# Kernel tuning notes

Hardware: AMD Instinct MI355X
Metric: run time of the kernel (lower is better)

## Reference

```python
import jax, jax.numpy as jnp
import numpy as np
from functools import partial

DN = ('NCHW', 'OIHW', 'NCHW')

def _conv(x, w):
    # 'same' conv, stride 1, NCHW
    return jax.lax.conv_general_dilated(x, w, window_strides=(1, 1),
                                        padding='SAME', dimension_numbers=DN)

def setup_inputs() -> dict:
    key = jax.random.key(0)
    ks = jax.random.split(key, 5)
    B, T, Cin, Oh, H, Wd = 8, 16, 64, 64, 56, 56
    x = jax.random.normal(ks[0], (B, T, Cin, H, Wd), dtype=jnp.float32)
    h = jax.random.normal(ks[1], (B, Oh, H, Wd), dtype=jnp.float32)
    # xavier-uniform-ish init scale for 3x3 kernels
    def xavier(k, shape):
        fan_in = shape[1] * shape[2] * shape[3]
        fan_out = shape[0] * shape[2] * shape[3]
        a = float(np.sqrt(6.0 / (fan_in + fan_out)))
        return jax.random.uniform(k, shape, dtype=jnp.float32, minval=-a, maxval=a)
    W = xavier(ks[2], (3 * Oh, Cin, 3, 3))  # [Wz; Wr; Wc]
    U = xavier(ks[3], (2 * Oh, Oh, 3, 3))   # [Uz; Ur]
    C = xavier(ks[4], (Oh, Oh, 3, 3))       # Uc (on r*h)
    return {"x": x, "h": h, "W": W, "U": U, "C": C}

def reference(x, h, W, U, C):
    Oh = C.shape[0]
    xt_major = jnp.swapaxes(x, 0, 1)  # [T, B, Cin, H, W]

    def step(h, xt):
        wx = _conv(xt, W)             # [B, 3*Oh, H, W]
        uh = _conv(h, U)              # [B, 2*Oh, H, W]
        z = jax.nn.sigmoid(wx[:, :Oh] + uh[:, :Oh])            # update gate
        r = jax.nn.sigmoid(wx[:, Oh:2 * Oh] + uh[:, Oh:2 * Oh])  # reset gate
        h_tilde = jnp.tanh(wx[:, 2 * Oh:] + _conv(r * h, C))
        h_new = (1.0 - z) * h + z * h_tilde
        return h_new, h_new

    h_last, outs = jax.lax.scan(step, h, xt_major)
    return jnp.swapaxes(outs, 0, 1), h_last  # [B, T, Oh, H, W], [B, Oh, H, W]
```

## Files before the change

### kernel.cpp

```cpp
#include <hip/hip_runtime.h>
#include <math.h>


#define PIX 4224
#define PIMG 244992
#define BIMG ((size_t)8 * PIMG)
#define WXS ((size_t)5505024)
#define HL_OFF ((size_t)25690112)
#define SLOT 2176

typedef unsigned short u16;
typedef __attribute__((ext_vector_type(8))) __bf16 bf16x8;
typedef __attribute__((ext_vector_type(4))) float f32x4;

__device__ __forceinline__ float bf2f(u16 u) {
  unsigned v = ((unsigned)u) << 16;
  float f;
  __builtin_memcpy(&f, &v, 4);
  return f;
}
__device__ __forceinline__ u16 f2bf(float f) {
  unsigned u;
  __builtin_memcpy(&u, &f, 4);
  u = (u + 0x7FFFu + ((u >> 16) & 1u)) >> 16;
  return (u16)u;
}
__device__ __forceinline__ void gll16(const u16* g, u16* l) {
  __builtin_amdgcn_global_load_lds(
      (const __attribute__((address_space(1))) void*)g,
      (__attribute__((address_space(3))) void*)l, 16, 0, 0);
}

__device__ __forceinline__ void stage_row(const u16* img, int prow, int x0,
                                          u16* ring, int slot, int lane,
                                          int wv) {
  const u16* g = img + (size_t)prow * PIX + x0 * 64;
  u16* l = ring + slot * SLOT;
  gll16(g + wv * 512 + lane * 8, l + wv * 512);
  if (wv == 0 && lane < 16) gll16(g + 2048 + lane * 8, l + 2048);
}

__device__ __forceinline__ void loadB18(const u16* wr, int NCH,
                                        bf16x8 (&B)[6][3]) {
#pragma unroll
  for (int p = 0; p < 6; ++p) {
    const int ky = p >> 1, kc = p & 1;
#pragma unroll
    for (int kx = 0; kx < 3; ++kx)
      B[p][kx] = *(const bf16x8*)(wr + (size_t)((ky * 3 + kx) * NCH) * 64 +
                                  kc * 32);
  }
}

__device__ __forceinline__ void conv_unit(const u16* ring, int rcb,
                                          const bf16x8 (&B)[6][3],
                                          f32x4 (&acc)[2], int lane) {
#pragma unroll
  for (int p = 0; p < 6; ++p) {
    const int ky = p >> 1, kc = p & 1;
    const int slot = (rcb + ky) & 7;
    bf16x8 af[2][3];
#pragma unroll
    for (int mf = 0; mf < 2; ++mf)
#pragma unroll
      for (int kx = 0; kx < 3; ++kx) {
        const int pp = mf * 16 + (lane & 15) + kx;
        const int sl = (kc * 4 + (lane >> 4)) ^ (pp & 7);
        af[mf][kx] = *(const bf16x8*)(ring + slot * SLOT + pp * 64 + sl * 8);
      }
#pragma unroll
    for (int kx = 0; kx < 3; ++kx)
#pragma unroll
      for (int mf = 0; mf < 2; ++mf)
        acc[mf] = __builtin_amdgcn_mfma_f32_16x16x32_bf16(af[mf][kx], B[p][kx],
                                                          acc[mf], 0, 0, 0);
  }
}

#define UNIT_SYNC() \
  asm volatile("s_waitcnt vmcnt(0)" ::: "memory"); \
  __syncthreads();

__device__ __forceinline__ void do_convW(const u16* __restrict__ xslot,
                                         const u16* __restrict__ wcat,
                                         u16* __restrict__ wx, int id,
                                         u16* ring) {
  const int ns = id / 112;
  const int rem = id % 112;
  const int b = rem & 7;
  const int v = rem >> 3;
  const int x0 = (v & 1) * 32;
  const int y0 = (v >> 1) * 8;
  const int lane = threadIdx.x & 63, wv = threadIdx.x >> 6;
  const int n0 = ns * 64 + wv * 16;

  const u16* wr = wcat + (size_t)(n0 + (lane & 15)) * 64 + (lane >> 4) * 8;
  bf16x8 B[6][3];
  loadB18(wr, 192, B);

  const u16* img = xslot + (size_t)b * PIMG;
#pragma unroll
  for (int k = 0; k < 3; ++k) stage_row(img, y0 + k, x0, ring, k, lane, wv);

  int S = 3;
#pragma unroll
  for (int u = 0; u < 8; ++u) {
    UNIT_SYNC();
    const int tgt = (u + 1 < 8) ? (u + 3) : 2;
#pragma unroll
    for (; S <= tgt; ++S)
      stage_row(img, y0 + S, x0, ring, S & 7, lane, wv);

    f32x4 acc[2] = {{0.f, 0.f, 0.f, 0.f}, {0.f, 0.f, 0.f, 0.f}};
    conv_unit(ring, u, B, acc, lane);

    const int y = y0 + u;
    const size_t rowb = ((size_t)(b * 56) + y) * 64;
    const int n = n0 + (lane & 15);
#pragma unroll
    for (int mf = 0; mf < 2; ++mf)
#pragma unroll
      for (int r = 0; r < 4; ++r) {
        const int px = x0 + mf * 16 + 4 * (lane >> 4) + r;
        wx[(rowb + px) * 192 + n] = f2bf(acc[mf][r]);
      }
  }
}

__device__ __forceinline__ void xprep_row(const float* __restrict__ x,
                                          u16* __restrict__ dst, int t, int b,
                                          int y, float (*tx)[57]) {
  const int tid = threadIdx.x;
  for (int i = tid; i < 64 * 56; i += 256) {
    int ci = i / 56, px = i % 56;
    tx[ci][px] = x[((size_t)(b * 16 + t) * 64 + ci) * 3136 + y * 56 + px];
  }
  __syncthreads();
  const size_t pb = (size_t)b * PIMG + (size_t)(y + 1) * PIX;
  for (int i = tid; i < 56 * 64; i += 256) {
    int px = i / 64, ci = i % 64;
    int gx = px + 1;
    dst[pb + gx * 64 + (((ci >> 3) ^ (gx & 7)) << 3) + (ci & 7)] =
        f2bf(tx[ci][px]);
  }
}

__global__ __launch_bounds__(256) void wprep_k(const float* __restrict__ W,
                                               const float* __restrict__ U,
                                               const float* __restrict__ C,
                                               u16* __restrict__ wcat) {
  int i = blockIdx.x * 256 + threadIdx.x;
  if (i >= 221184) return;
  float v;
  if (i < 110592) {
    int plane = i / 12288, rem = i % 12288, o = rem / 64, ci = rem % 64;
    v = W[(size_t)(o * 64 + ci) * 9 + plane];
  } else if (i < 184320) {
    int j = i - 110592;
    int plane = j / 8192, rem = j % 8192, o = rem / 64, ci = rem % 64;
    v = U[(size_t)(o * 64 + ci) * 9 + plane];
  } else {
    int j = i - 184320;
    int plane = j / 4096, rem = j % 4096, o = rem / 64, ci = rem % 64;
    v = C[(size_t)(o * 64 + ci) * 9 + plane];
  }
  wcat[i] = f2bf(v);
}

__global__ __launch_bounds__(256) void hinit_k(const float* __restrict__ h,
                                               u16* __restrict__ hpad,
                                               _Float16* __restrict__ hstate) {
  __shared__ float t[64][57];
  const int y = blockIdx.x, b = blockIdx.y;
  const int tid = threadIdx.x;
  for (int i = tid; i < 64 * 56; i += 256) {
    int ci = i / 56, xx = i % 56;
    t[ci][xx] = h[((size_t)(b * 64) + ci) * 3136 + y * 56 + xx];
  }
  __syncthreads();
  const size_t pb = (size_t)b * PIMG + (size_t)(y + 1) * PIX;
  const size_t sb = ((size_t)(b * 56) + y) * 64;
  for (int i = tid; i < 56 * 64; i += 256) {
    int px = i / 64, ci = i % 64;
    float v = t[ci][px];
    int gx = px + 1;
    hpad[pb + gx * 64 + (((ci >> 3) ^ (gx & 7)) << 3) + (ci & 7)] = f2bf(v);
    hstate[(sb + px) * 64 + ci] = (_Float16)v;
  }
}

__global__ __launch_bounds__(256) void xprep01_k(const float* __restrict__ x,
                                                 u16* __restrict__ x0,
                                                 u16* __restrict__ x1) {
  __shared__ float tt[64][57];
  const int t = blockIdx.y;
  xprep_row(x, t ? x1 : x0, t, blockIdx.x & 7, blockIdx.x >> 3, tt);
}

__global__ __launch_bounds__(256, 3) void convW0_k(const u16* __restrict__ xs,
                                                   const u16* __restrict__ wcat,
                                                   u16* __restrict__ wx) {
  __shared__ __align__(16) u16 ring[8 * SLOT];
  do_convW(xs, wcat, wx, blockIdx.x, ring);
}

__global__ __launch_bounds__(256, 3) void convUW_k(
    const u16* __restrict__ hpad, const u16* __restrict__ xpad_n,
    const u16* __restrict__ wcat, const u16* __restrict__ wx_c,
    u16* __restrict__ wx_n, _Float16* __restrict__ zbuf,
    u16* __restrict__ rhpad) {
  __shared__ __align__(16) u16 ring[8 * SLOT];
  const int bid = blockIdx.x;
  if (bid >= 448) {
    do_convW(xpad_n, wcat, wx_n, bid - 448, ring);
    return;
  }
  const int ns = bid / 224;
  const int rem = bid % 224;
  const int b = rem & 7;
  const int r2 = rem >> 3;
  const int x0 = (r2 & 1) * 32;
  const int y0 = (r2 >> 1) * 4;
  const int lane = threadIdx.x & 63, wv = threadIdx.x >> 6;
  const int n0 = ns * 64 + wv * 16;

  const u16* wr =
      wcat + 110592 + (size_t)(n0 + (lane & 15)) * 64 + (lane >> 4) * 8;
  bf16x8 B[6][3];
  loadB18(wr, 128, B);

  const u16* img = hpad + (size_t)b * PIMG;
#pragma unroll
  for (int k = 0; k < 3; ++k) stage_row(img, y0 + k, x0, ring, k, lane, wv);

  int S = 3;
#pragma unroll
  for (int u = 0; u < 4; ++u) {
    UNIT_SYNC();
    const int tgt = (u + 1 < 4) ? (u + 3) : 2;
#pragma unroll
    for (; S <= tgt; ++S)
      stage_row(img, y0 + S, x0, ring, S & 7, lane, wv);

    f32x4 acc[2] = {{0.f, 0.f, 0.f, 0.f}, {0.f, 0.f, 0.f, 0.f}};
    conv_unit(ring, u, B, acc, lane);

    const int y = y0 + u;
    const size_t rowb = ((size_t)(b * 56) + y) * 64;
    const int n = n0 + (lane & 15);
#pragma unroll
    for (int mf = 0; mf < 2; ++mf)
#pragma unroll
      for (int r = 0; r < 4; ++r) {
        const int px = x0 + mf * 16 + 4 * (lane >> 4) + r;
        if (px < 56) {
          const float a = bf2f(wx_c[(rowb + px) * 192 + n]) + acc[mf][r];
          const float s = 1.f / (1.f + __expf(-a));
          if (ns == 0) {
            zbuf[(rowb + px) * 64 + n] = (_Float16)s;
          } else {
            const int ci = n - 64;
            const int cp = mf * 16 + 4 * (lane >> 4) + r + 1;
            const int slotc = (u + 1) & 7;
            const float hv =
                bf2f(ring[slotc * SLOT + cp * 64 +
                          (((ci >> 3) ^ (cp & 7)) << 3) + (ci & 7)]);
            const int gx = px + 1;
            rhpad[(size_t)b * PIMG + (size_t)(y + 1) * PIX + gx * 64 +
                  (((ci >> 3) ^ (gx & 7)) << 3) + (ci & 7)] = f2bf(s * hv);
          }
        }
      }
  }
}

__global__ __launch_bounds__(256, 3) void convCX_k(
    const float* __restrict__ x, u16* __restrict__ xpad_w,
    const u16* __restrict__ rhpad, const u16* __restrict__ wcat,
    const u16* __restrict__ wx_c, const _Float16* __restrict__ zbuf,
    _Float16* __restrict__ hstate, u16* __restrict__ hpad,
    float* __restrict__ out, int t) {
  __shared__ __align__(16) u16 ring[8 * SLOT];
  __shared__ float ldt[4][16][33];
  const int bid = blockIdx.x;
  if (bid >= 448) {
    const int id = bid - 448;
    xprep_row(x, xpad_w, t + 2, id & 7, id >> 3, (float(*)[57])ring);
    return;
  }
  const int b = bid & 7;
  const int r2 = bid >> 3;
  const int x0 = (r2 & 1) * 32;
  const int y0 = (r2 >> 1) * 2;
  const int lane = threadIdx.x & 63, wv = threadIdx.x >> 6;
  const int n0 = wv * 16;

  const u16* wr =
      wcat + 184320 + (size_t)(n0 + (lane & 15)) * 64 + (lane >> 4) * 8;
  bf16x8 B[6][3];
  loadB18(wr, 64, B);

  const u16* img = rhpad + (size_t)b * PIMG;
#pragma unroll
  for (int k = 0; k < 3; ++k) stage_row(img, y0 + k, x0, ring, k, lane, wv);

#pragma unroll
  for (int u = 0; u < 2; ++u) {
    UNIT_SYNC();
    if (u == 0) stage_row(img, y0 + 3, x0, ring, 3, lane, wv);

    f32x4 acc[2] = {{0.f, 0.f, 0.f, 0.f}, {0.f, 0.f, 0.f, 0.f}};
    conv_unit(ring, u, B, acc, lane);

    const int y = y0 + u;
    const size_t rowb = ((size_t)(b * 56) + y) * 64;
    const int n = n0 + (lane & 15);
    float hnv[2][4];
#pragma unroll
    for (int mf = 0; mf < 2; ++mf)
#pragma unroll
      for (int r = 0; r < 4; ++r) {
        const int px = x0 + mf * 16 + 4 * (lane >> 4) + r;
        hnv[mf][r] = 0.f;
        if (px < 56) {
          const float a = bf2f(wx_c[(rowb + px) * 192 + 128 + n]) + acc[mf][r];
          const float htil = tanhf(a);
          const float z = (float)zbuf[(rowb + px) * 64 + n];
          const float ho = (float)hstate[(rowb + px) * 64 + n];
          const float hn = fmaf(z, htil - ho, ho);
          hstate[(rowb + px) * 64 + n] = (_Float16)hn;
          const int gx = px + 1;
          hpad[(size_t)b * PIMG + (size_t)(y + 1) * PIX + gx * 64 +
               (((n >> 3) ^ (gx & 7)) << 3) + (n & 7)] = f2bf(hn);
          hnv[mf][r] = hn;
        }
      }
    __syncthreads();
#pragma unroll
    for (int mf = 0; mf < 2; ++mf)
#pragma unroll
      for (int r = 0; r < 4; ++r)
        ldt[wv][lane & 15][mf * 16 + 4 * (lane >> 4) + r] = hnv[mf][r];
    __syncthreads();
    const int xl = lane & 31;
    const int px = x0 + xl;
    if (px < 56) {
#pragma unroll
      for (int cc = 0; cc < 8; ++cc) {
        const int ch = (lane >> 5) * 8 + cc;
        const float v = ldt[wv][ch][xl];
        out[(((size_t)(b * 16 + t)) * 64 + n0 + ch) * 3136 + y * 56 + px] = v;
        if (t == 15)
          out[HL_OFF + ((size_t)(b * 64) + n0 + ch) * 3136 + y * 56 + px] = v;
      }
    }
  }
}

extern "C" void kernel_launch(void* const* d_in, const int* in_sizes, int n_in,
                              void* d_out, int out_size, void* d_ws,
                              size_t ws_size, hipStream_t stream) {
  const float* x = (const float*)d_in[0];
  const float* h = (const float*)d_in[1];
  const float* W = (const float*)d_in[2];
  const float* U = (const float*)d_in[3];
  const float* C = (const float*)d_in[4];
  float* out = (float*)d_out;

  u16* ws_u = (u16*)d_ws;
  u16* xpad = ws_u;
  u16* hpad = xpad + 2 * BIMG;
  u16* rhpad = hpad + BIMG;
  u16* wcat = rhpad + BIMG;
  u16* wxr = wcat + 221184;
  _Float16* zbuf = (_Float16*)(wxr + 2 * WXS);
  _Float16* hstate = zbuf + 1835008;

  hipMemsetAsync(d_ws, 0, (size_t)4 * BIMG * sizeof(u16), stream);
  wprep_k<<<864, 256, 0, stream>>>(W, U, C, wcat);
  hinit_k<<<dim3(56, 8), 256, 0, stream>>>(h, hpad, hstate);
  xprep01_k<<<dim3(448, 2), 256, 0, stream>>>(x, xpad, xpad + BIMG);
  convW0_k<<<336, 256, 0, stream>>>(xpad, wcat, wxr);

  for (int t = 0; t < 16; ++t) {
    u16* xn = xpad + (size_t)((t + 1) & 1) * BIMG;
    u16* xw = xpad + (size_t)(t & 1) * BIMG;
    const u16* wxc = wxr + (size_t)(t & 1) * WXS;
    u16* wxn = wxr + (size_t)((t + 1) & 1) * WXS;

    const int nbA = 448 + ((t < 15) ? 336 : 0);
    convUW_k<<<nbA, 256, 0, stream>>>(hpad, xn, wcat, wxc, wxn, zbuf, rhpad);

    const int nbB = 448 + ((t < 14) ? 448 : 0);
    convCX_k<<<nbB, 256, 0, stream>>>(x, xw, rhpad, wcat, wxc, zbuf, hstate,
                                      hpad, out, t);
  }
}
```

Measured before the change: 813.7 us.

## Stage full padded rows and give each wave a 32x32 output tile

Conv blocks now stage whole padded image rows (both x halves) into a 4-slot LDS ring instead of half-width rows in an 8-slot ring. Each wave computes two 16-channel N fragments over a 32-pixel half, doubling the MFMA work per A-fragment load, and grid sizes are halved to match. The goal is to cut redundant halo loads and LDS A-fragment reads per MFMA. In exchange each wave holds twice as many weight registers, and occupancy drops to 2 blocks per CU with fewer blocks per launch. This could hurt latency hiding and SM fill, especially for the small convCX grid.

```diff
diff --git a/kernel.cpp b/kernel.cpp
--- a/kernel.cpp
+++ b/kernel.cpp
@@ -7,7 +7,7 @@
 #define BIMG ((size_t)8 * PIMG)
 #define WXS ((size_t)5505024)
 #define HL_OFF ((size_t)25690112)
-#define SLOT 2176
+#define SLOTW 4224
 
 typedef unsigned short u16;
 typedef __attribute__((ext_vector_type(8))) __bf16 bf16x8;
@@ -31,49 +31,54 @@
       (__attribute__((address_space(3))) void*)l, 16, 0, 0);
 }
 
-__device__ __forceinline__ void stage_row(const u16* img, int prow, int x0,
-                                          u16* ring, int slot, int lane,
-                                          int wv) {
-  const u16* g = img + (size_t)prow * PIX + x0 * 64;
-  u16* l = ring + slot * SLOT;
-  gll16(g + wv * 512 + lane * 8, l + wv * 512);
-  if (wv == 0 && lane < 16) gll16(g + 2048 + lane * 8, l + 2048);
-}
-
-__device__ __forceinline__ void loadB18(const u16* wr, int NCH,
-                                        bf16x8 (&B)[6][3]) {
+__device__ __forceinline__ void stage_rowf(const u16* img, int prow, u16* ring,
+                                           int slot, int lane, int wv) {
+  const u16* g = img + (size_t)prow * PIX;
+  u16* l = ring + slot * SLOTW;
+#pragma unroll
+  for (int c = wv; c < 8; c += 4) gll16(g + c * 512 + lane * 8, l + c * 512);
+  if (wv == 3 && lane < 16) gll16(g + 4096 + lane * 8, l + 4096);
+}
+
+__device__ __forceinline__ void loadB36(const u16* wr, int NCH,
+                                        bf16x8 (&B)[6][3][2]) {
 #pragma unroll
   for (int p = 0; p < 6; ++p) {
     const int ky = p >> 1, kc = p & 1;
 #pragma unroll
     for (int kx = 0; kx < 3; ++kx)
-      B[p][kx] = *(const bf16x8*)(wr + (size_t)((ky * 3 + kx) * NCH) * 64 +
-                                  kc * 32);
-  }
-}
-
-__device__ __forceinline__ void conv_unit(const u16* ring, int rcb,
-                                          const bf16x8 (&B)[6][3],
-                                          f32x4 (&acc)[2], int lane) {
+#pragma unroll
+      for (int nf = 0; nf < 2; ++nf)
+        B[p][kx][nf] = *(const bf16x8*)(wr + (size_t)((ky * 3 + kx) * NCH) * 64 +
+                                        nf * 1024 + kc * 32);
+  }
+}
+
+__device__ __forceinline__ void conv_unit2(const u16* ring, int rcb,
+                                           const bf16x8 (&B)[6][3][2],
+                                           f32x4 (&acc)[2][2], int lane,
+                                           int x0w) {
 #pragma unroll
   for (int p = 0; p < 6; ++p) {
     const int ky = p >> 1, kc = p & 1;
-    const int slot = (rcb + ky) & 7;
+    const int slot = (rcb + ky) & 3;
     bf16x8 af[2][3];
 #pragma unroll
     for (int mf = 0; mf < 2; ++mf)
 #pragma unroll
       for (int kx = 0; kx < 3; ++kx) {
-        const int pp = mf * 16 + (lane & 15) + kx;
+        const int pp = x0w + mf * 16 + (lane & 15) + kx;
         const int sl = (kc * 4 + (lane >> 4)) ^ (pp & 7);
-        af[mf][kx] = *(const bf16x8*)(ring + slot * SLOT + pp * 64 + sl * 8);
+        af[mf][kx] = *(const bf16x8*)(ring + slot * SLOTW + pp * 64 + sl * 8);
       }
 #pragma unroll
     for (int kx = 0; kx < 3; ++kx)
 #pragma unroll
       for (int mf = 0; mf < 2; ++mf)
-        acc[mf] = __builtin_amdgcn_mfma_f32_16x16x32_bf16(af[mf][kx], B[p][kx],
-                                                          acc[mf], 0, 0, 0);
+#pragma unroll
+        for (int nf = 0; nf < 2; ++nf)
+          acc[mf][nf] = __builtin_amdgcn_mfma_f32_16x16x32_bf16(
+              af[mf][kx], B[p][kx][nf], acc[mf][nf], 0, 0, 0);
   }
 }
 
@@ -85,44 +90,46 @@
                                          const u16* __restrict__ wcat,
                                          u16* __restrict__ wx, int id,
                                          u16* ring) {
-  const int ns = id / 112;
-  const int rem = id % 112;
+  const int ns = id / 56;
+  const int rem = id % 56;
   const int b = rem & 7;
-  const int v = rem >> 3;
-  const int x0 = (v & 1) * 32;
-  const int y0 = (v >> 1) * 8;
+  const int y0 = (rem >> 3) * 8;
   const int lane = threadIdx.x & 63, wv = threadIdx.x >> 6;
-  const int n0 = ns * 64 + wv * 16;
-
-  const u16* wr = wcat + (size_t)(n0 + (lane & 15)) * 64 + (lane >> 4) * 8;
-  bf16x8 B[6][3];
-  loadB18(wr, 192, B);
+  const int chs = wv & 1, x0w = (wv >> 1) * 32;
+  const int nb = ns * 64 + chs * 32;
+
+  const u16* wr = wcat + (size_t)(nb + (lane & 15)) * 64 + (lane >> 4) * 8;
+  bf16x8 B[6][3][2];
+  loadB36(wr, 192, B);
 
   const u16* img = xslot + (size_t)b * PIMG;
 #pragma unroll
-  for (int k = 0; k < 3; ++k) stage_row(img, y0 + k, x0, ring, k, lane, wv);
-
-  int S = 3;
+  for (int k = 0; k < 3; ++k) stage_rowf(img, y0 + k, ring, k, lane, wv);
+
 #pragma unroll
   for (int u = 0; u < 8; ++u) {
     UNIT_SYNC();
-    const int tgt = (u + 1 < 8) ? (u + 3) : 2;
-#pragma unroll
-    for (; S <= tgt; ++S)
-      stage_row(img, y0 + S, x0, ring, S & 7, lane, wv);
-
-    f32x4 acc[2] = {{0.f, 0.f, 0.f, 0.f}, {0.f, 0.f, 0.f, 0.f}};
-    conv_unit(ring, u, B, acc, lane);
+    if (u < 7) stage_rowf(img, y0 + u + 3, ring, (u + 3) & 3, lane, wv);
+
+    f32x4 acc[2][2];
+#pragma unroll
+    for (int mf = 0; mf < 2; ++mf)
+#pragma unroll
+      for (int nf = 0; nf < 2; ++nf) acc[mf][nf] = (f32x4){0.f, 0.f, 0.f, 0.f};
+    conv_unit2(ring, u, B, acc, lane, x0w);
 
     const int y = y0 + u;
     const size_t rowb = ((size_t)(b * 56) + y) * 64;
-    const int n = n0 + (lane & 15);
-#pragma unroll
-    for (int mf = 0; mf < 2; ++mf)
-#pragma unroll
-      for (int r = 0; r < 4; ++r) {
-        const int px = x0 + mf * 16 + 4 * (lane >> 4) + r;
-        wx[(rowb + px) * 192 + n] = f2bf(acc[mf][r]);
+#pragma unroll
+    for (int mf = 0; mf < 2; ++mf)
+#pragma unroll
+      for (int nf = 0; nf < 2; ++nf) {
+        const int n = nb + nf * 16 + (lane & 15);
+#pragma unroll
+        for (int r = 0; r < 4; ++r) {
+          const int px = x0w + mf * 16 + 4 * (lane >> 4) + r;
+          wx[(rowb + px) * 192 + n] = f2bf(acc[mf][nf][r]);
+        }
       }
   }
 }
@@ -197,161 +204,173 @@
   xprep_row(x, t ? x1 : x0, t, blockIdx.x & 7, blockIdx.x >> 3, tt);
 }
 
-__global__ __launch_bounds__(256, 3) void convW0_k(const u16* __restrict__ xs,
+__global__ __launch_bounds__(256, 2) void convW0_k(const u16* __restrict__ xs,
                                                    const u16* __restrict__ wcat,
                                                    u16* __restrict__ wx) {
-  __shared__ __align__(16) u16 ring[8 * SLOT];
+  __shared__ __align__(16) u16 ring[4 * SLOTW];
   do_convW(xs, wcat, wx, blockIdx.x, ring);
 }
 
-__global__ __launch_bounds__(256, 3) void convUW_k(
+__global__ __launch_bounds__(256, 2) void convUW_k(
     const u16* __restrict__ hpad, const u16* __restrict__ xpad_n,
     const u16* __restrict__ wcat, const u16* __restrict__ wx_c,
     u16* __restrict__ wx_n, _Float16* __restrict__ zbuf,
     u16* __restrict__ rhpad) {
-  __shared__ __align__(16) u16 ring[8 * SLOT];
+  __shared__ __align__(16) u16 ring[4 * SLOTW];
   const int bid = blockIdx.x;
-  if (bid >= 448) {
-    do_convW(xpad_n, wcat, wx_n, bid - 448, ring);
+  if (bid >= 224) {
+    do_convW(xpad_n, wcat, wx_n, bid - 224, ring);
     return;
   }
-  const int ns = bid / 224;
-  const int rem = bid % 224;
+  const int ns = bid / 112;
+  const int rem = bid % 112;
   const int b = rem & 7;
-  const int r2 = rem >> 3;
-  const int x0 = (r2 & 1) * 32;
-  const int y0 = (r2 >> 1) * 4;
+  const int y0 = (rem >> 3) * 4;
   const int lane = threadIdx.x & 63, wv = threadIdx.x >> 6;
-  const int n0 = ns * 64 + wv * 16;
+  const int chs = wv & 1, x0w = (wv >> 1) * 32;
+  const int nb = ns * 64 + chs * 32;
 
   const u16* wr =
-      wcat + 110592 + (size_t)(n0 + (lane & 15)) * 64 + (lane >> 4) * 8;
-  bf16x8 B[6][3];
-  loadB18(wr, 128, B);
+      wcat + 110592 + (size_t)(nb + (lane & 15)) * 64 + (lane >> 4) * 8;
+  bf16x8 B[6][3][2];
+  loadB36(wr, 128, B);
 
   const u16* img = hpad + (size_t)b * PIMG;
 #pragma unroll
-  for (int k = 0; k < 3; ++k) stage_row(img, y0 + k, x0, ring, k, lane, wv);
-
-  int S = 3;
+  for (int k = 0; k < 3; ++k) stage_rowf(img, y0 + k, ring, k, lane, wv);
+
 #pragma unroll
   for (int u = 0; u < 4; ++u) {
     UNIT_SYNC();
-    const int tgt = (u + 1 < 4) ? (u + 3) : 2;
-#pragma unroll
-    for (; S <= tgt; ++S)
-      stage_row(img, y0 + S, x0, ring, S & 7, lane, wv);
-
-    f32x4 acc[2] = {{0.f, 0.f, 0.f, 0.f}, {0.f, 0.f, 0.f, 0.f}};
-    conv_unit(ring, u, B, acc, lane);
+    if (u < 3) stage_rowf(img, y0 + u + 3, ring, (u + 3) & 3, lane, wv);
+
+    f32x4 acc[2][2];
+#pragma unroll
+    for (int mf = 0; mf < 2; ++mf)
+#pragma unroll
+      for (int nf = 0; nf < 2; ++nf) acc[mf][nf] = (f32x4){0.f, 0.f, 0.f, 0.f};
+    conv_unit2(ring, u, B, acc, lane, x0w);
 
     const int y = y0 + u;
     const size_t rowb = ((size_t)(b * 56) + y) * 64;
-    const int n = n0 + (lane & 15);
-#pragma unroll
-    for (int mf = 0; mf < 2; ++mf)
-#pragma unroll
-      for (int r = 0; r < 4; ++r) {
-        const int px = x0 + mf * 16 + 4 * (lane >> 4) + r;
-        if (px < 56) {
-          const float a = bf2f(wx_c[(rowb + px) * 192 + n]) + acc[mf][r];
-          const float s = 1.f / (1.f + __expf(-a));
-          if (ns == 0) {
-            zbuf[(rowb + px) * 64 + n] = (_Float16)s;
-          } else {
-            const int ci = n - 64;
-            const int cp = mf * 16 + 4 * (lane >> 4) + r + 1;
-            const int slotc = (u + 1) & 7;
-            const float hv =
-                bf2f(ring[slotc * SLOT + cp * 64 +
-                          (((ci >> 3) ^ (cp & 7)) << 3) + (ci & 7)]);
-            const int gx = px + 1;
-            rhpad[(size_t)b * PIMG + (size_t)(y + 1) * PIX + gx * 64 +
-                  (((ci >> 3) ^ (gx & 7)) << 3) + (ci & 7)] = f2bf(s * hv);
+#pragma unroll
+    for (int mf = 0; mf < 2; ++mf)
+#pragma unroll
+      for (int nf = 0; nf < 2; ++nf) {
+        const int n = nb + nf * 16 + (lane & 15);
+        const int cl = chs * 32 + nf * 16 + (lane & 15);
+#pragma unroll
+        for (int r = 0; r < 4; ++r) {
+          const int px = x0w + mf * 16 + 4 * (lane >> 4) + r;
+          if (px < 56) {
+            const float a = bf2f(wx_c[(rowb + px) * 192 + n]) + acc[mf][nf][r];
+            const float s = 1.f / (1.f + __expf(-a));
+            if (ns == 0) {
+              zbuf[(rowb + px) * 64 + cl] = (_Float16)s;
+            } else {
+              const int cp = px + 1;
+              const int slotc = (u + 1) & 3;
+              const float hv =
+                  bf2f(ring[slotc * SLOTW + cp * 64 +
+                            (((cl >> 3) ^ (cp & 7)) << 3) + (cl & 7)]);
+              rhpad[(size_t)b * PIMG + (size_t)(y + 1) * PIX + cp * 64 +
+                    (((cl >> 3) ^ (cp & 7)) << 3) + (cl & 7)] = f2bf(s * hv);
+            }
           }
         }
       }
   }
 }
 
-__global__ __launch_bounds__(256, 3) void convCX_k(
+__global__ __launch_bounds__(256, 2) void convCX_k(
     const float* __restrict__ x, u16* __restrict__ xpad_w,
     const u16* __restrict__ rhpad, const u16* __restrict__ wcat,
     const u16* __restrict__ wx_c, const _Float16* __restrict__ zbuf,
     _Float16* __restrict__ hstate, u16* __restrict__ hpad,
     float* __restrict__ out, int t) {
-  __shared__ __align__(16) u16 ring[8 * SLOT];
-  __shared__ float ldt[4][16][33];
+  __shared__ __align__(16) u16 ring[4 * SLOTW];
+  __shared__ float ldt[4][32][33];
   const int bid = blockIdx.x;
-  if (bid >= 448) {
-    const int id = bid - 448;
+  if (bid >= 112) {
+    const int id = bid - 112;
     xprep_row(x, xpad_w, t + 2, id & 7, id >> 3, (float(*)[57])ring);
     return;
   }
   const int b = bid & 7;
-  const int r2 = bid >> 3;
-  const int x0 = (r2 & 1) * 32;
-  const int y0 = (r2 >> 1) * 2;
+  const int y0 = (bid >> 3) * 4;
   const int lane = threadIdx.x & 63, wv = threadIdx.x >> 6;
-  const int n0 = wv * 16;
+  const int chs = wv & 1, x0w = (wv >> 1) * 32;
+  const int nb = chs * 32;
 
   const u16* wr =
-      wcat + 184320 + (size_t)(n0 + (lane & 15)) * 64 + (lane >> 4) * 8;
-  bf16x8 B[6][3];
-  loadB18(wr, 64, B);
+      wcat + 184320 + (size_t)(nb + (lane & 15)) * 64 + (lane >> 4) * 8;
+  bf16x8 B[6][3][2];
+  loadB36(wr, 64, B);
 
   const u16* img = rhpad + (size_t)b * PIMG;
 #pragma unroll
-  for (int k = 0; k < 3; ++k) stage_row(img, y0 + k, x0, ring, k, lane, wv);
-
-#pragma unroll
-  for (int u = 0; u < 2; ++u) {
+  for (int k = 0; k < 3; ++k) stage_rowf(img, y0 + k, ring, k, lane, wv);
+
+#pragma unroll
+  for (int u = 0; u < 4; ++u) {
     UNIT_SYNC();
-    if (u == 0) stage_row(img, y0 + 3, x0, ring, 3, lane, wv);
-
-    f32x4 acc[2] = {{0.f, 0.f, 0.f, 0.f}, {0.f, 0.f, 0.f, 0.f}};
-    conv_unit(ring, u, B, acc, lane);
+    if (u < 3) stage_rowf(img, y0 + u + 3, ring, (u + 3) & 3, lane, wv);
+
+    f32x4 acc[2][2];
+#pragma unroll
+    for (int mf = 0; mf < 2; ++mf)
+#pragma unroll
+      for (int nf = 0; nf < 2; ++nf) acc[mf][nf] = (f32x4){0.f, 0.f, 0.f, 0.f};
+    conv_unit2(ring, u, B, acc, lane, x0w);
 
     const int y = y0 + u;
     const size_t rowb = ((size_t)(b * 56) + y) * 64;
-    const int n = n0 + (lane & 15);
-    float hnv[2][4];
-#pragma unroll
-    for (int mf = 0; mf < 2; ++mf)
-#pragma unroll
-      for (int r = 0; r < 4; ++r) {
-        const int px = x0 + mf * 16 + 4 * (lane >> 4) + r;
-        hnv[mf][r] = 0.f;
-        if (px < 56) {
-          const float a = bf2f(wx_c[(rowb + px) * 192 + 128 + n]) + acc[mf][r];
-          const float htil = tanhf(a);
-          const float z = (float)zbuf[(rowb + px) * 64 + n];
-          const float ho = (float)hstate[(rowb + px) * 64 + n];
-          const float hn = fmaf(z, htil - ho, ho);
-          hstate[(rowb + px) * 64 + n] = (_Float16)hn;
-          const int gx = px + 1;
-          hpad[(size_t)b * PIMG + (size_t)(y + 1) * PIX + gx * 64 +
-               (((n >> 3) ^ (gx & 7)) << 3) + (n & 7)] = f2bf(hn);
-          hnv[mf][r] = hn;
+    float hnv[2][2][4];
+#pragma unroll
+    for (int mf = 0; mf < 2; ++mf)
+#pragma unroll
+      for (int nf = 0; nf < 2; ++nf) {
+        const int n = nb + nf * 16 + (lane & 15);
+#pragma unroll
+        for (int r = 0; r < 4; ++r) {
+          const int px = x0w + mf * 16 + 4 * (lane >> 4) + r;
+          hnv[mf][nf][r] = 0.f;
+          if (px < 56) {
+            const float a =
+                bf2f(wx_c[(rowb + px) * 192 + 128 + n]) + acc[mf][nf][r];
+            const float htil = tanhf(a);
+            const float z = (float)zbuf[(rowb + px) * 64 + n];
+            const float ho = (float)hstate[(rowb + px) * 64 + n];
+            const float hn = fmaf(z, htil - ho, ho);
+            hstate[(rowb + px) * 64 + n] = (_Float16)hn;
+            const int gx = px + 1;
+            hpad[(size_t)b * PIMG + (size_t)(y + 1) * PIX + gx * 64 +
+                 (((n >> 3) ^ (gx & 7)) << 3) + (n & 7)] = f2bf(hn);
+            hnv[mf][nf][r] = hn;
+          }
         }
       }
     __syncthreads();
 #pragma unroll
     for (int mf = 0; mf < 2; ++mf)
 #pragma unroll
-      for (int r = 0; r < 4; ++r)
-        ldt[wv][lane & 15][mf * 16 + 4 * (lane >> 4) + r] = hnv[mf][r];
+      for (int nf = 0; nf < 2; ++nf)
+#pragma unroll
+        for (int r = 0; r < 4; ++r)
+          ldt[wv][nf * 16 + (lane & 15)][mf * 16 + 4 * (lane >> 4) + r] =
+              hnv[mf][nf][r];
     __syncthreads();
     const int xl = lane & 31;
-    const int px = x0 + xl;
+    const int px = x0w + xl;
     if (px < 56) {
 #pragma unroll
-      for (int cc = 0; cc < 8; ++cc) {
-        const int ch = (lane >> 5) * 8 + cc;
+      for (int cc = 0; cc < 16; ++cc) {
+        const int ch = (lane >> 5) * 16 + cc;
         const float v = ldt[wv][ch][xl];
-        out[(((size_t)(b * 16 + t)) * 64 + n0 + ch) * 3136 + y * 56 + px] = v;
+        const int oc = nb + ch;
+        out[(((size_t)(b * 16 + t)) * 64 + oc) * 3136 + y * 56 + px] = v;
         if (t == 15)
-          out[HL_OFF + ((size_t)(b * 64) + n0 + ch) * 3136 + y * 56 + px] = v;
+          out[HL_OFF + ((size_t)(b * 64) + oc) * 3136 + y * 56 + px] = v;
       }
     }
   }
@@ -380,7 +399,7 @@
   wprep_k<<<864, 256, 0, stream>>>(W, U, C, wcat);
   hinit_k<<<dim3(56, 8), 256, 0, stream>>>(h, hpad, hstate);
   xprep01_k<<<dim3(448, 2), 256, 0, stream>>>(x, xpad, xpad + BIMG);
-  convW0_k<<<336, 256, 0, stream>>>(xpad, wcat, wxr);
+  convW0_k<<<168, 256, 0, stream>>>(xpad, wcat, wxr);
 
   for (int t = 0; t < 16; ++t) {
     u16* xn = xpad + (size_t)((t + 1) & 1) * BIMG;
@@ -388,10 +407,10 @@
     const u16* wxc = wxr + (size_t)(t & 1) * WXS;
     u16* wxn = wxr + (size_t)((t + 1) & 1) * WXS;
 
-    const int nbA = 448 + ((t < 15) ? 336 : 0);
+    const int nbA = 224 + ((t < 15) ? 168 : 0);
     convUW_k<<<nbA, 256, 0, stream>>>(hpad, xn, wcat, wxc, wxn, zbuf, rhpad);
 
-    const int nbB = 448 + ((t < 14) ? 448 : 0);
+    const int nbB = 112 + ((t < 14) ? 448 : 0);
     convCX_k<<<nbB, 256, 0, stream>>>(x, xw, rhpad, wcat, wxc, zbuf, hstate,
                                       hpad, out, t);
   }
```

Measured after the change: 1.414 ms. 1.74x slower.

## Stage conv epilogue outputs through LDS for coalesced 16-byte global stores

Applied to the files above, without the earlier changes.

Conv epilogues now write their per-lane results into a shared-memory tile and then issue one coalesced 16-byte store per thread. This replaces the scattered 2-byte stores to wx, zbuf, rhpad, hstate and hpad. The W-conv blocks are also split into 4-row units, doubling their block count, to match the other conv blocks. In exchange each block uses more LDS and adds an extra barrier per row. Padded columns now get zeros written, which keeps the padding intact.

```diff
diff --git a/kernel.cpp b/kernel.cpp
--- a/kernel.cpp
+++ b/kernel.cpp
@@ -12,6 +12,7 @@
 typedef unsigned short u16;
 typedef __attribute__((ext_vector_type(8))) __bf16 bf16x8;
 typedef __attribute__((ext_vector_type(4))) float f32x4;
+typedef __attribute__((ext_vector_type(4))) unsigned int u32x4;
 
 __device__ __forceinline__ float bf2f(u16 u) {
   unsigned v = ((unsigned)u) << 16;
@@ -24,6 +25,12 @@
   __builtin_memcpy(&u, &f, 4);
   u = (u + 0x7FFFu + ((u >> 16) & 1u)) >> 16;
   return (u16)u;
+}
+__device__ __forceinline__ u16 f2h(float f) {
+  _Float16 h = (_Float16)f;
+  u16 u;
+  __builtin_memcpy(&u, &h, 2);
+  return u;
 }
 __device__ __forceinline__ void gll16(const u16* g, u16* l) {
   __builtin_amdgcn_global_load_lds(
@@ -84,17 +91,18 @@
 __device__ __forceinline__ void do_convW(const u16* __restrict__ xslot,
                                          const u16* __restrict__ wcat,
                                          u16* __restrict__ wx, int id,
-                                         u16* ring) {
-  const int ns = id / 112;
-  const int rem = id % 112;
+                                         u16* ring, u16* tile) {
+  const int ns = id / 224;
+  const int rem = id % 224;
   const int b = rem & 7;
   const int v = rem >> 3;
   const int x0 = (v & 1) * 32;
-  const int y0 = (v >> 1) * 8;
+  const int y0 = (v >> 1) * 4;
   const int lane = threadIdx.x & 63, wv = threadIdx.x >> 6;
-  const int n0 = ns * 64 + wv * 16;
-
-  const u16* wr = wcat + (size_t)(n0 + (lane & 15)) * 64 + (lane >> 4) * 8;
+  const int nl = wv * 16 + (lane & 15);
+
+  const u16* wr =
+      wcat + (size_t)(ns * 64 + nl) * 64 + (lane >> 4) * 8;
   bf16x8 B[6][3];
   loadB18(wr, 192, B);
 
@@ -102,28 +110,29 @@
 #pragma unroll
   for (int k = 0; k < 3; ++k) stage_row(img, y0 + k, x0, ring, k, lane, wv);
 
-  int S = 3;
-#pragma unroll
-  for (int u = 0; u < 8; ++u) {
+#pragma unroll
+  for (int u = 0; u < 4; ++u) {
     UNIT_SYNC();
-    const int tgt = (u + 1 < 8) ? (u + 3) : 2;
-#pragma unroll
-    for (; S <= tgt; ++S)
-      stage_row(img, y0 + S, x0, ring, S & 7, lane, wv);
+    if (u < 3) stage_row(img, y0 + u + 3, x0, ring, (u + 3) & 7, lane, wv);
 
     f32x4 acc[2] = {{0.f, 0.f, 0.f, 0.f}, {0.f, 0.f, 0.f, 0.f}};
     conv_unit(ring, u, B, acc, lane);
 
     const int y = y0 + u;
     const size_t rowb = ((size_t)(b * 56) + y) * 64;
-    const int n = n0 + (lane & 15);
 #pragma unroll
     for (int mf = 0; mf < 2; ++mf)
 #pragma unroll
       for (int r = 0; r < 4; ++r) {
-        const int px = x0 + mf * 16 + 4 * (lane >> 4) + r;
-        wx[(rowb + px) * 192 + n] = f2bf(acc[mf][r]);
+        const int pl = mf * 16 + 4 * (lane >> 4) + r;
+        tile[pl * 64 + nl] = f2bf(acc[mf][r]);
       }
+    __syncthreads();
+    {
+      const int c = threadIdx.x, pl = c >> 3, off = c & 7;
+      *(u32x4*)(wx + (rowb + x0 + pl) * 192 + ns * 64 + off * 8) =
+          *(const u32x4*)(tile + pl * 64 + off * 8);
+    }
   }
 }
 
@@ -201,7 +210,8 @@
                                                    const u16* __restrict__ wcat,
                                                    u16* __restrict__ wx) {
   __shared__ __align__(16) u16 ring[8 * SLOT];
-  do_convW(xs, wcat, wx, blockIdx.x, ring);
+  __shared__ __align__(16) u16 tile[32 * 64];
+  do_convW(xs, wcat, wx, blockIdx.x, ring, tile);
 }
 
 __global__ __launch_bounds__(256, 3) void convUW_k(
@@ -210,9 +220,10 @@
     u16* __restrict__ wx_n, _Float16* __restrict__ zbuf,
     u16* __restrict__ rhpad) {
   __shared__ __align__(16) u16 ring[8 * SLOT];
+  __shared__ __align__(16) u16 tile[32 * 64];
   const int bid = blockIdx.x;
   if (bid >= 448) {
-    do_convW(xpad_n, wcat, wx_n, bid - 448, ring);
+    do_convW(xpad_n, wcat, wx_n, bid - 448, ring, tile);
     return;
   }
   const int ns = bid / 224;
@@ -222,10 +233,11 @@
   const int x0 = (r2 & 1) * 32;
   const int y0 = (r2 >> 1) * 4;
   const int lane = threadIdx.x & 63, wv = threadIdx.x >> 6;
-  const int n0 = ns * 64 + wv * 16;
+  const int nl = wv * 16 + (lane & 15);
+  const int n = ns * 64 + nl;
 
   const u16* wr =
-      wcat + 110592 + (size_t)(n0 + (lane & 15)) * 64 + (lane >> 4) * 8;
+      wcat + 110592 + (size_t)n * 64 + (lane >> 4) * 8;
   bf16x8 B[6][3];
   loadB18(wr, 128, B);
 
@@ -233,44 +245,43 @@
 #pragma unroll
   for (int k = 0; k < 3; ++k) stage_row(img, y0 + k, x0, ring, k, lane, wv);
 
-  int S = 3;
 #pragma unroll
   for (int u = 0; u < 4; ++u) {
     UNIT_SYNC();
-    const int tgt = (u + 1 < 4) ? (u + 3) : 2;
-#pragma unroll
-    for (; S <= tgt; ++S)
-      stage_row(img, y0 + S, x0, ring, S & 7, lane, wv);
+    if (u < 3) stage_row(img, y0 + u + 3, x0, ring, (u + 3) & 7, lane, wv);
 
     f32x4 acc[2] = {{0.f, 0.f, 0.f, 0.f}, {0.f, 0.f, 0.f, 0.f}};
     conv_unit(ring, u, B, acc, lane);
 
     const int y = y0 + u;
     const size_t rowb = ((size_t)(b * 56) + y) * 64;
-    const int n = n0 + (lane & 15);
 #pragma unroll
     for (int mf = 0; mf < 2; ++mf)
 #pragma unroll
       for (int r = 0; r < 4; ++r) {
-        const int px = x0 + mf * 16 + 4 * (lane >> 4) + r;
-        if (px < 56) {
-          const float a = bf2f(wx_c[(rowb + px) * 192 + n]) + acc[mf][r];
-          const float s = 1.f / (1.f + __expf(-a));
-          if (ns == 0) {
-            zbuf[(rowb + px) * 64 + n] = (_Float16)s;
-          } else {
-            const int ci = n - 64;
-            const int cp = mf * 16 + 4 * (lane >> 4) + r + 1;
-            const int slotc = (u + 1) & 7;
-            const float hv =
-                bf2f(ring[slotc * SLOT + cp * 64 +
-                          (((ci >> 3) ^ (cp & 7)) << 3) + (ci & 7)]);
-            const int gx = px + 1;
-            rhpad[(size_t)b * PIMG + (size_t)(y + 1) * PIX + gx * 64 +
-                  (((ci >> 3) ^ (gx & 7)) << 3) + (ci & 7)] = f2bf(s * hv);
-          }
+        const int pl = mf * 16 + 4 * (lane >> 4) + r;
+        const int pg = x0 + pl;
+        const float a = bf2f(wx_c[(rowb + pg) * 192 + n]) + acc[mf][r];
+        const float s = 1.f / (1.f + __expf(-a));
+        if (ns == 0) {
+          tile[pl * 64 + nl] = f2h(s);
+        } else {
+          const int cp = pl + 1;
+          const int sw = (((nl >> 3) ^ (cp & 7)) << 3) | (nl & 7);
+          const float hv = bf2f(ring[((u + 1) & 7) * SLOT + cp * 64 + sw]);
+          tile[pl * 64 + sw] = f2bf((pg < 56) ? s * hv : 0.f);
         }
       }
+    __syncthreads();
+    {
+      const int c = threadIdx.x, pl = c >> 3, off = c & 7;
+      const u32x4 vv = *(const u32x4*)(tile + pl * 64 + off * 8);
+      if (ns == 0)
+        *(u32x4*)((u16*)zbuf + (rowb + x0 + pl) * 64 + off * 8) = vv;
+      else
+        *(u32x4*)(rhpad + (size_t)b * PIMG + (size_t)(y + 1) * PIX +
+                  (x0 + pl + 1) * 64 + off * 8) = vv;
+    }
   }
 }
 
@@ -282,6 +293,8 @@
     float* __restrict__ out, int t) {
   __shared__ __align__(16) u16 ring[8 * SLOT];
   __shared__ float ldt[4][16][33];
+  __shared__ __align__(16) u16 th[32 * 64];
+  __shared__ __align__(16) u16 tp[32 * 64];
   const int bid = blockIdx.x;
   if (bid >= 448) {
     const int id = bid - 448;
@@ -293,10 +306,10 @@
   const int x0 = (r2 & 1) * 32;
   const int y0 = (r2 >> 1) * 2;
   const int lane = threadIdx.x & 63, wv = threadIdx.x >> 6;
-  const int n0 = wv * 16;
+  const int nl = wv * 16 + (lane & 15);
 
   const u16* wr =
-      wcat + 184320 + (size_t)(n0 + (lane & 15)) * 64 + (lane >> 4) * 8;
+      wcat + 184320 + (size_t)nl * 64 + (lane >> 4) * 8;
   bf16x8 B[6][3];
   loadB18(wr, 64, B);
 
@@ -314,34 +327,32 @@
 
     const int y = y0 + u;
     const size_t rowb = ((size_t)(b * 56) + y) * 64;
-    const int n = n0 + (lane & 15);
-    float hnv[2][4];
 #pragma unroll
     for (int mf = 0; mf < 2; ++mf)
 #pragma unroll
       for (int r = 0; r < 4; ++r) {
-        const int px = x0 + mf * 16 + 4 * (lane >> 4) + r;
-        hnv[mf][r] = 0.f;
-        if (px < 56) {
-          const float a = bf2f(wx_c[(rowb + px) * 192 + 128 + n]) + acc[mf][r];
-          const float htil = tanhf(a);
-          const float z = (float)zbuf[(rowb + px) * 64 + n];
-          const float ho = (float)hstate[(rowb + px) * 64 + n];
-          const float hn = fmaf(z, htil - ho, ho);
-          hstate[(rowb + px) * 64 + n] = (_Float16)hn;
-          const int gx = px + 1;
-          hpad[(size_t)b * PIMG + (size_t)(y + 1) * PIX + gx * 64 +
-               (((n >> 3) ^ (gx & 7)) << 3) + (n & 7)] = f2bf(hn);
-          hnv[mf][r] = hn;
-        }
+        const int pl = mf * 16 + 4 * (lane >> 4) + r;
+        const int pg = x0 + pl;
+        const float a = bf2f(wx_c[(rowb + pg) * 192 + 128 + nl]) + acc[mf][r];
+        const float htil = tanhf(a);
+        const float z = (float)zbuf[(rowb + pg) * 64 + nl];
+        const float ho = (float)hstate[(rowb + pg) * 64 + nl];
+        float hn = fmaf(z, htil - ho, ho);
+        hn = (pg < 56) ? hn : 0.f;
+        th[pl * 64 + nl] = f2h(hn);
+        const int cp = pl + 1;
+        tp[pl * 64 + ((((nl >> 3) ^ (cp & 7)) << 3) | (nl & 7))] = f2bf(hn);
+        ldt[wv][lane & 15][pl] = hn;
       }
     __syncthreads();
-#pragma unroll
-    for (int mf = 0; mf < 2; ++mf)
-#pragma unroll
-      for (int r = 0; r < 4; ++r)
-        ldt[wv][lane & 15][mf * 16 + 4 * (lane >> 4) + r] = hnv[mf][r];
-    __syncthreads();
+    {
+      const int c = threadIdx.x, pl = c >> 3, off = c & 7;
+      *(u32x4*)((u16*)hstate + (rowb + x0 + pl) * 64 + off * 8) =
+          *(const u32x4*)(th + pl * 64 + off * 8);
+      *(u32x4*)(hpad + (size_t)b * PIMG + (size_t)(y + 1) * PIX +
+                (x0 + pl + 1) * 64 + off * 8) =
+          *(const u32x4*)(tp + pl * 64 + off * 8);
+    }
     const int xl = lane & 31;
     const int px = x0 + xl;
     if (px < 56) {
@@ -349,9 +360,10 @@
       for (int cc = 0; cc < 8; ++cc) {
         const int ch = (lane >> 5) * 8 + cc;
         const float v = ldt[wv][ch][xl];
-        out[(((size_t)(b * 16 + t)) * 64 + n0 + ch) * 3136 + y * 56 + px] = v;
+        const int oc = wv * 16 + ch;
+        out[(((size_t)(b * 16 + t)) * 64 + oc) * 3136 + y * 56 + px] = v;
         if (t == 15)
-          out[HL_OFF + ((size_t)(b * 64) + n0 + ch) * 3136 + y * 56 + px] = v;
+          out[HL_OFF + ((size_t)(b * 64) + oc) * 3136 + y * 56 + px] = v;
       }
     }
   }
@@ -380,7 +392,7 @@
   wprep_k<<<864, 256, 0, stream>>>(W, U, C, wcat);
   hinit_k<<<dim3(56, 8), 256, 0, stream>>>(h, hpad, hstate);
   xprep01_k<<<dim3(448, 2), 256, 0, stream>>>(x, xpad, xpad + BIMG);
-  convW0_k<<<336, 256, 0, stream>>>(xpad, wcat, wxr);
+  convW0_k<<<672, 256, 0, stream>>>(xpad, wcat, wxr);
 
   for (int t = 0; t < 16; ++t) {
     u16* xn = xpad + (size_t)((t + 1) & 1) * BIMG;
@@ -388,7 +400,7 @@
     const u16* wxc = wxr + (size_t)(t & 1) * WXS;
     u16* wxn = wxr + (size_t)((t + 1) & 1) * WXS;
 
-    const int nbA = 448 + ((t < 15) ? 336 : 0);
+    const int nbA = 448 + ((t < 15) ? 672 : 0);
     convUW_k<<<nbA, 256, 0, stream>>>(hpad, xn, wcat, wxc, wxn, zbuf, rhpad);
 
     const int nbB = 448 + ((t < 14) ? 448 : 0);
```

New measurement: 830.0 us. 2.0% more time.
